# Performance work log

Hardware: AMD Instinct MI355X
Metric: run time of the kernel (lower is better)

The kernel has to match this reference:

```python
import jax, jax.numpy as jnp
import numpy as np

B, S, D, H = 2, 2048, 1024, 16
HD = D // H
EPS = 1e-5


def layer_norm(x, g, b):
    m = jnp.mean(x, axis=-1, keepdims=True)
    v = jnp.mean(jnp.square(x - m), axis=-1, keepdims=True)
    return (x - m) * jax.lax.rsqrt(v + EPS) * g + b


def setup_inputs() -> dict:
    key = jax.random.key(0)
    ks = jax.random.split(key, 16)
    s = 0.02
    x = jax.random.normal(ks[0], (B, S, D), dtype=jnp.float32)
    mask = jax.random.randint(ks[1], (1, 1, S, S), 0, 2, dtype=jnp.int32)
    return {
        "x": x,
        "mask": mask,
        "Wq": jax.random.normal(ks[2], (D, D), jnp.float32) * s,
        "Wk": jax.random.normal(ks[3], (D, D), jnp.float32) * s,
        "Wv": jax.random.normal(ks[4], (D, D), jnp.float32) * s,
        "Wo": jax.random.normal(ks[5], (D, D), jnp.float32) * s,
        "bo": jax.random.normal(ks[6], (D,), jnp.float32) * s,
        "ln1_g": jnp.ones((D,), jnp.float32),
        "ln1_b": jnp.zeros((D,), jnp.float32),
        "W1": jax.random.normal(ks[7], (D, 4 * D), jnp.float32) * s,
        "b1": jax.random.normal(ks[8], (4 * D,), jnp.float32) * s,
        "W2": jax.random.normal(ks[9], (4 * D, D), jnp.float32) * s,
        "b2": jax.random.normal(ks[10], (D,), jnp.float32) * s,
        "ln2_g": jnp.ones((D,), jnp.float32),
        "ln2_b": jnp.zeros((D,), jnp.float32),
    }


def reference(x, mask, Wq, Wk, Wv, Wo, bo, ln1_g, ln1_b, W1, b1, W2, b2, ln2_g, ln2_b):
    # --- multi-head attention (dropout = identity in eval) ---
    q = (x @ Wq).reshape(B, S, H, HD)
    k = (x @ Wk).reshape(B, S, H, HD)
    v = (x @ Wv).reshape(B, S, H, HD)
    scores = jnp.einsum("bshd,bthd->bhst", q, k) / jnp.sqrt(jnp.float32(HD))
    scores = jnp.where(mask == 1, jnp.float32(-1e9), scores)
    p = jax.nn.softmax(scores, axis=-1)
    o = jnp.einsum("bhst,bthd->bshd", p, v).reshape(B, S, D)
    attn_out = o @ Wo + bo
    # --- residual with norm on the branch (note: norm applied to attn output) ---
    x = x + layer_norm(attn_out, ln1_g, ln1_b)
    # --- FFN: gelu after fc1 AND after fc2 (as in source) ---
    h = jax.nn.gelu(x @ W1 + b1, approximate=False)
    h = jax.nn.gelu(h @ W2 + b2, approximate=False)
    x = x + layer_norm(h, ln2_g, ln2_b)
    return x
```

## Files before the change

kernel.cpp:

```cpp
#include <hip/hip_runtime.h>
#include <hip/hip_bf16.h>
#include <cstdint>

#define BB 2
#define SS 2048
#define DD 1024
#define HH 16
#define HDIM 64
#define MROWS (BB*SS)

typedef __bf16 bf16;
using bf16x8 = __bf16 __attribute__((ext_vector_type(8)));
using bf16x4 = __bf16 __attribute__((ext_vector_type(4)));
using bf16x2 = __bf16 __attribute__((ext_vector_type(2)));
using f32x4  = float __attribute__((ext_vector_type(4)));

__device__ __forceinline__ float gelu_exact(float x) {
    return 0.5f * x * (1.f + erff(x * 0.70710678118654752f));
}

__device__ __forceinline__ void stage16(const bf16* g, bf16* lds_chunk_base, int lane) {
#if __has_builtin(__builtin_amdgcn_global_load_lds)
    __builtin_amdgcn_global_load_lds((const __attribute__((address_space(1))) void*)g,
                                     (__attribute__((address_space(3))) void*)lds_chunk_base,
                                     16, 0, 0);
#else
    *(bf16x8*)(lds_chunk_base + lane * 8) = *(const bf16x8*)g;
#endif
}

__device__ __forceinline__ unsigned lds_addr(const void* p) {
    return (unsigned)(uintptr_t)(const __attribute__((address_space(3))) void*)p;
}

__device__ __forceinline__ bf16x8 dsr(unsigned addr) {
    bf16x8 r;
    asm volatile("ds_read_b128 %0, %1" : "=v"(r) : "v"(addr));
    return r;
}

__global__ __launch_bounds__(256) void prep_kernel(
    const float* __restrict__ x, bf16* __restrict__ x_b,
    const int* __restrict__ mask, unsigned long long* __restrict__ maskb,
    const float* __restrict__ Wq, const float* __restrict__ Wk,
    const float* __restrict__ Wv, const float* __restrict__ Wo,
    const float* __restrict__ W1, const float* __restrict__ W2,
    bf16* __restrict__ Wqkv_t, bf16* __restrict__ Wo_t,
    bf16* __restrict__ W1_t, bf16* __restrict__ W2_t) {
    const int bid = blockIdx.x;
    if (bid < 4096) {
        int i = bid * 256 + threadIdx.x;
        float4 v = ((const float4*)x)[i];
        bf16x4 o;
        o[0] = (bf16)v.x; o[1] = (bf16)v.y; o[2] = (bf16)v.z; o[3] = (bf16)v.w;
        *(bf16x4*)(x_b + (size_t)i * 4) = o;
        return;
    }
    if (bid < 20480) {
        int gid = (bid - 4096) * 256 + threadIdx.x;
        int mv = mask[gid];
        unsigned long long bal = __ballot(mv == 1);
        if ((threadIdx.x & 63) == 0) maskb[gid >> 6] = bal;
        return;
    }
    int t = bid - 20480;
    const float* W; bf16* Wt; int K, N, bx, by;
    if (t < 4096) {
        int wsel = t >> 10;
        int tt = t & 1023;
        W  = (wsel == 0) ? Wq : (wsel == 1) ? Wk : (wsel == 2) ? Wv : Wo;
        Wt = (wsel == 3) ? Wo_t : (Wqkv_t + (size_t)wsel * 1024 * 1024);
        K = 1024; N = 1024; bx = (tt & 31) * 32; by = (tt >> 5) * 32;
    } else if (t < 8192) {
        int tt = t - 4096;
        W = W1; Wt = W1_t; K = 1024; N = 4096;
        bx = (tt & 127) * 32; by = (tt >> 7) * 32;
    } else {
        int tt = t - 8192;
        W = W2; Wt = W2_t; K = 4096; N = 1024;
        bx = (tt & 31) * 32; by = (tt >> 5) * 32;
    }
    __shared__ float tile[32][33];
    int tx = threadIdx.x & 31;
    int ty = threadIdx.x >> 5;
#pragma unroll
    for (int j = 0; j < 4; ++j)
        tile[ty + j * 8][tx] = W[(size_t)(by + ty + j * 8) * N + bx + tx];
    __syncthreads();
#pragma unroll
    for (int j = 0; j < 4; ++j)
        Wt[(size_t)(bx + ty + j * 8) * K + by + tx] = (bf16)tile[tx][ty + j * 8];
}

template <int EPI>
__global__ __launch_bounds__(256, 2) void gemm_bt(const bf16* __restrict__ A,
                                                  const bf16* __restrict__ Bt,
                                                  void* __restrict__ C,
                                                  void* __restrict__ C2,
                                                  const float* __restrict__ bias,
                                                  int M, int N, int K, int ldk) {
    __shared__ __align__(16) bf16 As[128 * 64];
    __shared__ __align__(16) bf16 Bs[128 * 64];
    const int tid  = threadIdx.x;
    const int lane = tid & 63;
    const int wave = tid >> 6;
    const int l16  = lane & 15;
    const int quad = lane >> 4;
    const int wm = wave >> 1, wn = wave & 1;

    int bx, by, bz;
    {
        const int Gx = gridDim.x, Gy = gridDim.y, Gz = gridDim.z;
        const int nwg = Gx * Gy * Gz;
        int L = blockIdx.x + Gx * (blockIdx.y + Gy * blockIdx.z);
        if ((nwg & 7) == 0) {
            int chunk = nwg >> 3;
            L = (L & 7) * chunk + (L >> 3);
        }
        bx = L % Gx; int rest = L / Gx; by = rest % Gy; bz = rest / Gy;
    }
    const int m0 = by * 128, n0 = bx * 128;
    const int z  = bz;
    A  += (size_t)z * K;
    Bt += (size_t)z * K;

    f32x4 acc[4][4];
#pragma unroll
    for (int i = 0; i < 4; ++i)
#pragma unroll
        for (int j = 0; j < 4; ++j) acc[i][j] = (f32x4){0.f, 0.f, 0.f, 0.f};

    const int nsteps = K >> 6;
    for (int kt = 0; kt < nsteps; ++kt) {
        const int kbase = kt << 6;
#pragma unroll
        for (int c = 0; c < 4; ++c) {
            int chunk = wave * 4 + c;
            int gi = chunk * 64 + lane;
            int m  = gi >> 3;
            int cp = gi & 7;
            int g  = cp ^ (m & 7);
            stage16(A  + (size_t)(m0 + m) * ldk + kbase + g * 8, As + chunk * 512, lane);
            stage16(Bt + (size_t)(n0 + m) * ldk + kbase + g * 8, Bs + chunk * 512, lane);
        }
        __syncthreads();
#pragma unroll
        for (int ks = 0; ks < 2; ++ks) {
            bf16x8 af[4], bfr[4];
#pragma unroll
            for (int i = 0; i < 4; ++i) {
                int m = wm * 64 + i * 16 + l16;
                int g = ks * 4 + quad;
                af[i]  = *(const bf16x8*)(As + m * 64 + ((g ^ (m & 7)) * 8));
                int n = wn * 64 + i * 16 + l16;
                bfr[i] = *(const bf16x8*)(Bs + n * 64 + ((g ^ (n & 7)) * 8));
            }
#pragma unroll
            for (int i = 0; i < 4; ++i)
#pragma unroll
                for (int j = 0; j < 4; ++j)
                    acc[i][j] = __builtin_amdgcn_mfma_f32_16x16x32_bf16(af[i], bfr[j], acc[i][j], 0, 0, 0);
        }
        __syncthreads();
    }

    float* Cz = (EPI == 4) ? (z ? (float*)C2 : (float*)C) : nullptr;
#pragma unroll
    for (int i = 0; i < 4; ++i) {
        int row = m0 + wm * 64 + i * 16 + quad * 4;
#pragma unroll
        for (int j = 0; j < 4; ++j) {
            int col = n0 + wn * 64 + j * 16 + l16;
            float bv = (EPI == 2) ? bias[col] : 0.f;
#pragma unroll
            for (int r = 0; r < 4; ++r) {
                float v = acc[i][j][r];
                if (EPI == 2) v = gelu_exact(v + bv);
                size_t idx = (size_t)(row + r) * N + col;
                if (EPI == 4) Cz[idx] = v;
                else          ((bf16*)C)[idx] = (bf16)v;
            }
        }
    }
}

template <int EPI>
__global__ __launch_bounds__(512, 2) void gemm256(const bf16* __restrict__ A,
                                                  const bf16* __restrict__ Bt,
                                                  void* __restrict__ C0, void* __restrict__ C1,
                                                  void* __restrict__ C2v, void* __restrict__ C3,
                                                  const float* __restrict__ bias,
                                                  int M, int N, int K, int ldk) {
    __shared__ __align__(16) bf16 As[2 * 16384];
    __shared__ __align__(16) bf16 Bs[2 * 16384];
    const int tid  = threadIdx.x;
    const int lane = tid & 63;
    const int wave = tid >> 6;
    const int l16  = lane & 15;
    const int quad = lane >> 4;
    const int wm = wave >> 2;
    const int wn = wave & 3;

    int bx, by, bz;
    {
        const int Gx = gridDim.x, Gy = gridDim.y, Gz = gridDim.z;
        const int nwg = Gx * Gy * Gz;
        int L = blockIdx.x + Gx * (blockIdx.y + Gy * blockIdx.z);
        if ((nwg & 7) == 0) {
            int chunk = nwg >> 3;
            L = (L & 7) * chunk + (L >> 3);
        }
        bx = L % Gx; int rest = L / Gx; by = rest % Gy; bz = rest / Gy;
    }
    const int m0 = by * 256, n0 = bx * 256;
    const int z  = bz;
    A  += (size_t)z * K;
    Bt += (size_t)z * K;

    const int grow = wave * 8 + (lane >> 3);
    const int gg   = (lane & 7) ^ (grow & 7);
    const bf16* sA = A  + (size_t)(m0 + grow) * ldk + gg * 8;
    const bf16* sB = Bt + (size_t)(n0 + grow) * ldk + gg * 8;
    const int dchunk = wave * 512;

    const unsigned s7 = (unsigned)(l16 & 7);
    const unsigned e0 = ((unsigned)quad ^ s7) * 16;
    const unsigned arow0 = (unsigned)(wm * 128 + l16) * 128;
    const unsigned brow0 = (unsigned)(wn * 64 + l16) * 128;
    const unsigned asBase = lds_addr(As);
    const unsigned bsBase = lds_addr(Bs);

    f32x4 acc[8][4];
#pragma unroll
    for (int i = 0; i < 8; ++i)
#pragma unroll
        for (int j = 0; j < 4; ++j) acc[i][j] = (f32x4){0.f, 0.f, 0.f, 0.f};

    const int nt = K >> 6;

    auto stageHalf = [&](int t, int R0, bool isB) {
        const int kb = t << 6;
        const bf16* s = isB ? sB : sA;
        bf16* d = (isB ? Bs : As) + (t & 1) * 16384 + R0 * 64 + dchunk;
        stage16(s + (size_t)R0 * ldk + kb, d, lane);
        stage16(s + (size_t)(R0 + 64) * ldk + kb, d + 4096, lane);
    };

    stageHalf(0, 0, false); stageHalf(0, 128, false);
    stageHalf(0, 0, true);  stageHalf(0, 128, true);
    if (1 < nt) {
        stageHalf(1, 0, false);
        asm volatile("s_waitcnt vmcnt(2)");
    } else {
        asm volatile("s_waitcnt vmcnt(0)");
    }
    __builtin_amdgcn_s_barrier();

    for (int t = 0; t < nt; ++t) {
        const unsigned ab = asBase + (unsigned)(t & 1) * 32768 + arow0;
        const unsigned bb = bsBase + (unsigned)(t & 1) * 32768 + brow0;
        bf16x8 af[4][2], b0[2][2], b1[2][2];

#pragma unroll
        for (int i = 0; i < 4; ++i) {
            af[i][0] = dsr(ab + i * 2048 + e0);
            af[i][1] = dsr(ab + i * 2048 + (e0 ^ 64));
        }
#pragma unroll
        for (int j = 0; j < 2; ++j) {
            b0[j][0] = dsr(bb + j * 2048 + e0);
            b0[j][1] = dsr(bb + j * 2048 + (e0 ^ 64));
        }
        if (t + 1 < nt) { stageHalf(t + 1, 128, false); stageHalf(t + 1, 0, true); }
        __builtin_amdgcn_s_barrier();
        asm volatile("s_waitcnt lgkmcnt(0)");
        __builtin_amdgcn_sched_barrier(0);
        __builtin_amdgcn_s_setprio(1);
#pragma unroll
        for (int i = 0; i < 4; ++i)
#pragma unroll
            for (int j = 0; j < 2; ++j)
#pragma unroll
                for (int kk = 0; kk < 2; ++kk)
                    acc[i][j] = __builtin_amdgcn_mfma_f32_16x16x32_bf16(af[i][kk], b0[j][kk], acc[i][j], 0, 0, 0);
        __builtin_amdgcn_s_setprio(0);
        __builtin_amdgcn_s_barrier();

#pragma unroll
        for (int j = 0; j < 2; ++j) {
            b1[j][0] = dsr(bb + 4096 + j * 2048 + e0);
            b1[j][1] = dsr(bb + 4096 + j * 2048 + (e0 ^ 64));
        }
        if (t + 1 < nt) stageHalf(t + 1, 128, true);
        __builtin_amdgcn_s_barrier();
        asm volatile("s_waitcnt lgkmcnt(0)");
        __builtin_amdgcn_sched_barrier(0);
        __builtin_amdgcn_s_setprio(1);
#pragma unroll
        for (int i = 0; i < 4; ++i)
#pragma unroll
            for (int j = 0; j < 2; ++j)
#pragma unroll
                for (int kk = 0; kk < 2; ++kk)
                    acc[i][j + 2] = __builtin_amdgcn_mfma_f32_16x16x32_bf16(af[i][kk], b1[j][kk], acc[i][j + 2], 0, 0, 0);
        __builtin_amdgcn_s_setprio(0);
        __builtin_amdgcn_s_barrier();

#pragma unroll
        for (int i = 0; i < 4; ++i) {
            af[i][0] = dsr(ab + 8192 + i * 2048 + e0);
            af[i][1] = dsr(ab + 8192 + i * 2048 + (e0 ^ 64));
        }
        __builtin_amdgcn_s_barrier();
        asm volatile("s_waitcnt lgkmcnt(0)");
        __builtin_amdgcn_sched_barrier(0);
        __builtin_amdgcn_s_setprio(1);
#pragma unroll
        for (int i = 0; i < 4; ++i)
#pragma unroll
            for (int j = 0; j < 2; ++j)
#pragma unroll
                for (int kk = 0; kk < 2; ++kk)
                    acc[i + 4][j + 2] = __builtin_amdgcn_mfma_f32_16x16x32_bf16(af[i][kk], b1[j][kk], acc[i + 4][j + 2], 0, 0, 0);
        __builtin_amdgcn_s_setprio(0);
        __builtin_amdgcn_s_barrier();

        if (t + 2 < nt) stageHalf(t + 2, 0, false);
        __builtin_amdgcn_s_barrier();
        __builtin_amdgcn_s_setprio(1);
#pragma unroll
        for (int i = 0; i < 4; ++i)
#pragma unroll
            for (int j = 0; j < 2; ++j)
#pragma unroll
                for (int kk = 0; kk < 2; ++kk)
                    acc[i + 4][j] = __builtin_amdgcn_mfma_f32_16x16x32_bf16(af[i][kk], b0[j][kk], acc[i + 4][j], 0, 0, 0);
        __builtin_amdgcn_s_setprio(0);
        if (t + 2 < nt) { asm volatile("s_waitcnt vmcnt(2)"); }
        else            { asm volatile("s_waitcnt vmcnt(0)"); }
        __builtin_amdgcn_s_barrier();
    }

    float* Cz = nullptr;
    if (EPI == 4) Cz = (z == 0) ? (float*)C0 : (z == 1) ? (float*)C1 : (z == 2) ? (float*)C2v : (float*)C3;
#pragma unroll
    for (int i = 0; i < 8; ++i) {
        int row = m0 + wm * 128 + i * 16 + quad * 4;
#pragma unroll
        for (int j = 0; j < 4; ++j) {
            int col = n0 + wn * 64 + j * 16 + l16;
            float bv = (EPI == 2) ? bias[col] : 0.f;
#pragma unroll
            for (int r = 0; r < 4; ++r) {
                float v = acc[i][j][r];
                if (EPI == 2) v = gelu_exact(v + bv);
                size_t idx = (size_t)(row + r) * N + col;
                if (EPI == 4) Cz[idx] = v;
                else          ((bf16*)C0)[idx] = (bf16)v;
            }
        }
    }
}

__global__ __launch_bounds__(512, 2) void flash_attn(const bf16* __restrict__ qkv,
                                                     const unsigned long long* __restrict__ maskb,
                                                     bf16* __restrict__ o) {
    __shared__ __align__(16) bf16 Ks[128 * 64];
    __shared__ __align__(16) bf16 Vts[64 * 136];
    const int tid  = threadIdx.x;
    const int lane = tid & 63;
    const int wave = tid >> 6;
    const int l16  = lane & 15;
    const int quad = lane >> 4;

    int bqx, bhy;
    {
        const int Gx = gridDim.x, Gy = gridDim.y;
        int L = blockIdx.x + Gx * blockIdx.y;
        int chunk = (Gx * Gy) >> 3;
        L = (L & 7) * chunk + (L >> 3);
        bqx = L % Gx; bhy = L / Gx;
    }
    const int bh = bhy;
    const int b = bh >> 4, h = bh & 15;
    const int q0 = bqx * 128;
    const size_t rowb = (size_t)b * SS;
    const float SCL = 0.18033688011112042f;

    const size_t qrow = (rowb + q0 + wave * 16 + l16) * 3072 + h * 64;
    bf16x8 qf[2];
    {
        bf16x8 q0r = *(const bf16x8*)(qkv + qrow + quad * 8);
        bf16x8 q1r = *(const bf16x8*)(qkv + qrow + 32 + quad * 8);
#pragma unroll
        for (int j = 0; j < 8; ++j) {
            qf[0][j] = (bf16)((float)q0r[j] * SCL);
            qf[1][j] = (bf16)((float)q1r[j] * SCL);
        }
    }

    f32x4 oacc[4];
#pragma unroll
    for (int d = 0; d < 4; ++d) oacc[d] = (f32x4){0.f, 0.f, 0.f, 0.f};
    f32x4 lacc = (f32x4){0.f, 0.f, 0.f, 0.f};
    const int mrow32 = (q0 + wave * 16 + l16) * 32;

    bf16x8 ones;
#pragma unroll
    for (int j = 0; j < 8; ++j) ones[j] = (bf16)1.0f;

    const int vt_tc = (lane >> 4) * 32 + ((lane >> 1) & 3) * 8 + ((lane >> 3) & 1) * 4 + 2 * (lane & 1);
    const int vd8 = wave * 8;

    int kst[2], ksg[2];
#pragma unroll
    for (int c = 0; c < 2; ++c) {
        int gi = (wave * 2 + c) * 64 + lane;
        kst[c] = gi >> 3;
        ksg[c] = (gi & 7) ^ (kst[c] & 7);
    }

    bf16x8 kreg[2], vreg[2];
    ulonglong2 mwreg;
#pragma unroll
    for (int c = 0; c < 2; ++c)
        kreg[c] = *(const bf16x8*)(qkv + (rowb + kst[c]) * 3072 + 1024 + h * 64 + ksg[c] * 8);
    {
        const bf16* vg = qkv + (rowb + 2 * lane) * 3072 + 2048 + h * 64 + vd8;
        vreg[0] = *(const bf16x8*)(vg);
        vreg[1] = *(const bf16x8*)(vg + 3072);
    }
    mwreg = *(const ulonglong2*)(maskb + mrow32);

    for (int kt = 0; kt < SS / 128; ++kt) {
        __syncthreads();
#pragma unroll
        for (int c = 0; c < 2; ++c)
            *(bf16x8*)(Ks + (wave * 2 + c) * 512 + lane * 8) = kreg[c];
#pragma unroll
        for (int j = 0; j < 8; ++j) {
            bf16x2 pr; pr[0] = vreg[0][j]; pr[1] = vreg[1][j];
            *(bf16x2*)(Vts + (vd8 + j) * 136 + vt_tc) = pr;
        }
        ulonglong2 mw = mwreg;
        __syncthreads();

        if (kt + 1 < SS / 128) {
            const int t0n = (kt + 1) * 128;
#pragma unroll
            for (int c = 0; c < 2; ++c)
                kreg[c] = *(const bf16x8*)(qkv + (rowb + t0n + kst[c]) * 3072 + 1024 + h * 64 + ksg[c] * 8);
            {
                const bf16* vg = qkv + (rowb + t0n + 2 * lane) * 3072 + 2048 + h * 64 + vd8;
                vreg[0] = *(const bf16x8*)(vg);
                vreg[1] = *(const bf16x8*)(vg + 3072);
            }
            mwreg = *(const ulonglong2*)(maskb + mrow32 + (kt + 1) * 2);
        }

        f32x4 st[8];
        __builtin_amdgcn_s_setprio(1);
#pragma unroll
        for (int tg = 0; tg < 8; ++tg) {
            int tl = tg * 16 + l16;
            bf16x8 a0 = *(const bf16x8*)(Ks + tl * 64 + ((quad       ^ (tl & 7)) * 8));
            bf16x8 a1 = *(const bf16x8*)(Ks + tl * 64 + (((4 + quad) ^ (tl & 7)) * 8));
            f32x4 s = (f32x4){0.f, 0.f, 0.f, 0.f};
            s = __builtin_amdgcn_mfma_f32_16x16x32_bf16(a0, qf[0], s, 0, 0, 0);
            s = __builtin_amdgcn_mfma_f32_16x16x32_bf16(a1, qf[1], s, 0, 0, 0);
            st[tg] = s;
        }
        __builtin_amdgcn_s_setprio(0);

        unsigned long long s0 = mw.x >> (quad * 4);
        unsigned long long s1 = mw.y >> (quad * 4);
        bf16x8 pva[4];
#pragma unroll
        for (int tg = 0; tg < 8; ++tg) {
            unsigned int bits = (unsigned int)(((tg < 4) ? s0 : s1) >> ((tg & 3) * 16));
#pragma unroll
            for (int r = 0; r < 4; ++r) {
                float p = __builtin_amdgcn_exp2f(st[tg][r]);
                p = ((bits >> r) & 1u) ? 0.f : p;
                pva[tg >> 1][(tg & 1) * 4 + r] = (bf16)p;
            }
        }

        __builtin_amdgcn_s_setprio(1);
#pragma unroll
        for (int kc = 0; kc < 4; ++kc) {
#pragma unroll
            for (int dg = 0; dg < 4; ++dg) {
                bf16x8 bfrag = *(const bf16x8*)(Vts + (dg * 16 + l16) * 136 + kc * 32 + quad * 8);
                oacc[dg] = __builtin_amdgcn_mfma_f32_16x16x32_bf16(pva[kc], bfrag, oacc[dg], 0, 0, 0);
            }
            lacc = __builtin_amdgcn_mfma_f32_16x16x32_bf16(pva[kc], ones, lacc, 0, 0, 0);
        }
        __builtin_amdgcn_s_setprio(0);
    }

#pragma unroll
    for (int r = 0; r < 4; ++r) {
        float inv_l = 1.f / lacc[r];
        bf16* orow = o + (rowb + q0 + wave * 16 + quad * 4 + r) * DD + h * 64;
#pragma unroll
        for (int dg = 0; dg < 4; ++dg)
            orow[dg * 16 + l16] = (bf16)(oacc[dg][r] * inv_l);
    }
}

template <bool GELU, bool WB16, int NP>
__global__ __launch_bounds__(256) void ln_fused(const float* __restrict__ resid,
                                                const float* __restrict__ p0,
                                                const float* __restrict__ p1,
                                                const float* __restrict__ p2,
                                                const float* __restrict__ p3,
                                                const float* __restrict__ bias,
                                                const float* __restrict__ g,
                                                const float* __restrict__ bb,
                                                float* __restrict__ outf,
                                                bf16* __restrict__ outb) {
    const int row = blockIdx.x;
    const int tid = threadIdx.x;
    const size_t base = (size_t)row * DD + tid * 4;
    float4 a0 = *(const float4*)(p0 + base);
    float4 a1 = *(const float4*)(p1 + base);
    float4 bz = *(const float4*)(bias + tid * 4);
    float ax = a0.x + a1.x + bz.x;
    float ay = a0.y + a1.y + bz.y;
    float az = a0.z + a1.z + bz.z;
    float aw = a0.w + a1.w + bz.w;
    if (NP == 4) {
        float4 a2 = *(const float4*)(p2 + base);
        float4 a3 = *(const float4*)(p3 + base);
        ax += a2.x + a3.x; ay += a2.y + a3.y; az += a2.z + a3.z; aw += a2.w + a3.w;
    }
    if (GELU) { ax = gelu_exact(ax); ay = gelu_exact(ay); az = gelu_exact(az); aw = gelu_exact(aw); }
    float s1 = ax + ay + az + aw;
    float s2 = ax * ax + ay * ay + az * az + aw * aw;
#pragma unroll
    for (int off = 32; off; off >>= 1) {
        s1 += __shfl_xor(s1, off, 64);
        s2 += __shfl_xor(s2, off, 64);
    }
    __shared__ float red[8];
    if ((tid & 63) == 0) { red[(tid >> 6) * 2] = s1; red[(tid >> 6) * 2 + 1] = s2; }
    __syncthreads();
    s1 = red[0] + red[2] + red[4] + red[6];
    s2 = red[1] + red[3] + red[5] + red[7];
    float mean = s1 * (1.f / DD);
    float var  = s2 * (1.f / DD) - mean * mean;
    float rs = rsqrtf(var + 1e-5f);
    float4 gv = *(const float4*)(g + tid * 4);
    float4 bv = *(const float4*)(bb + tid * 4);
    float4 rv = *(const float4*)(resid + base);
    float y0 = rv.x + (ax - mean) * rs * gv.x + bv.x;
    float y1 = rv.y + (ay - mean) * rs * gv.y + bv.y;
    float y2 = rv.z + (az - mean) * rs * gv.z + bv.z;
    float y3 = rv.w + (aw - mean) * rs * gv.w + bv.w;
    float4 yo = make_float4(y0, y1, y2, y3);
    *(float4*)(outf + base) = yo;
    if (WB16) {
        bf16x4 ob;
        ob[0] = (bf16)y0; ob[1] = (bf16)y1; ob[2] = (bf16)y2; ob[3] = (bf16)y3;
        *(bf16x4*)(outb + base) = ob;
    }
}

extern "C" void kernel_launch(void* const* d_in, const int* in_sizes, int n_in,
                              void* d_out, int out_size, void* d_ws, size_t ws_size,
                              hipStream_t stream) {
    const float* x    = (const float*)d_in[0];
    const int*   mask = (const int*)d_in[1];
    const float* Wq   = (const float*)d_in[2];
    const float* Wk   = (const float*)d_in[3];
    const float* Wv   = (const float*)d_in[4];
    const float* Wo   = (const float*)d_in[5];
    const float* bo   = (const float*)d_in[6];
    const float* ln1g = (const float*)d_in[7];
    const float* ln1b = (const float*)d_in[8];
    const float* W1   = (const float*)d_in[9];
    const float* b1   = (const float*)d_in[10];
    const float* W2   = (const float*)d_in[11];
    const float* b2   = (const float*)d_in[12];
    const float* ln2g = (const float*)d_in[13];
    const float* ln2b = (const float*)d_in[14];

    char* w = (char*)d_ws;
    bf16* Wqkv_t = (bf16*)w; w += (size_t)3072 * 1024 * 2;
    bf16* Wo_t   = (bf16*)w; w += (size_t)1024 * 1024 * 2;
    bf16* W1_t   = (bf16*)w; w += (size_t)4096 * 1024 * 2;
    bf16* W2_t   = (bf16*)w; w += (size_t)1024 * 4096 * 2;
    bf16* x_b    = (bf16*)w; w += (size_t)MROWS * DD * 2;
    bf16* qkv    = (bf16*)w; w += (size_t)MROWS * 3072 * 2;
    float* R     = (float*)w; w += (size_t)MROWS * DD * 8;
    float* x1_f  = (float*)w; w += (size_t)MROWS * DD * 4;
    unsigned long long* maskb = (unsigned long long*)w; w += (size_t)SS * 32 * 8;
    bf16* o_b  = x_b;
    bf16* x1_b = x_b;
    float* op0 = R;
    float* op1 = R + (size_t)MROWS * DD;
    bf16*  h_b = (bf16*)R;
    float* fp0 = (float*)d_out;
    float* fp1 = (float*)x_b;
    float* fp2 = (float*)x_b + (size_t)4 * 1024 * 1024;
    float* fp3 = (float*)d_ws;

    prep_kernel<<<32768, 256, 0, stream>>>(x, x_b, mask, maskb,
                                           Wq, Wk, Wv, Wo, W1, W2,
                                           Wqkv_t, Wo_t, W1_t, W2_t);

    gemm256<0><<<dim3(12, 16, 1), 512, 0, stream>>>(x_b, Wqkv_t, qkv, nullptr, nullptr, nullptr, nullptr, MROWS, 3072, 1024, 1024);
    flash_attn<<<dim3(SS / 128, BB * HH), 512, 0, stream>>>(qkv, maskb, o_b);
    gemm_bt<4><<<dim3(8, 32, 2), 256, 0, stream>>>(o_b, Wo_t, op0, op1, nullptr, MROWS, 1024, 512, 1024);
    ln_fused<false, true, 2><<<MROWS, 256, 0, stream>>>(x, op0, op1, nullptr, nullptr, bo, ln1g, ln1b, x1_f, x1_b);
    gemm256<2><<<dim3(16, 16, 1), 512, 0, stream>>>(x1_b, W1_t, h_b, nullptr, nullptr, nullptr, b1, MROWS, 4096, 1024, 1024);
    gemm256<4><<<dim3(4, 16, 4), 512, 0, stream>>>(h_b, W2_t, fp0, fp1, fp2, fp3, nullptr, MROWS, 1024, 1024, 4096);
    ln_fused<true, false, 4><<<MROWS, 256, 0, stream>>>(x1_f, fp0, fp1, fp2, fp3, b2, ln2g, ln2b, (float*)d_out, nullptr);
}
```

Before: 369.4 us.

## Double-buffer K/V shared memory tiles in flash attention to drop a barrier

Gives the K and transposed-V shared tiles two buffers. While computing on tile kt, the kernel writes tile kt+1 into the other buffer and issues global loads for tile kt+2. This cuts the two block barriers per iteration down to one and overlaps the shared-memory stores with compute. In exchange, shared memory per block roughly doubles, which may lower occupancy at 2 blocks of 512 threads per CU, and the loaded register tiles now stay live for longer.

```diff
diff --git a/kernel.cpp b/kernel.cpp
--- a/kernel.cpp
+++ b/kernel.cpp
@@ -365,8 +365,8 @@
 __global__ __launch_bounds__(512, 2) void flash_attn(const bf16* __restrict__ qkv,
                                                      const unsigned long long* __restrict__ maskb,
                                                      bf16* __restrict__ o) {
-    __shared__ __align__(16) bf16 Ks[128 * 64];
-    __shared__ __align__(16) bf16 Vts[64 * 136];
+    __shared__ __align__(16) bf16 Ks[2 * 128 * 64];
+    __shared__ __align__(16) bf16 Vts[2 * 64 * 136];
     const int tid  = threadIdx.x;
     const int lane = tid & 63;
     const int wave = tid >> 6;
@@ -422,49 +422,52 @@
 
     bf16x8 kreg[2], vreg[2];
     ulonglong2 mwreg;
-#pragma unroll
-    for (int c = 0; c < 2; ++c)
-        kreg[c] = *(const bf16x8*)(qkv + (rowb + kst[c]) * 3072 + 1024 + h * 64 + ksg[c] * 8);
-    {
-        const bf16* vg = qkv + (rowb + 2 * lane) * 3072 + 2048 + h * 64 + vd8;
+    auto loadKV = [&](int t0) {
+#pragma unroll
+        for (int c = 0; c < 2; ++c)
+            kreg[c] = *(const bf16x8*)(qkv + (rowb + t0 + kst[c]) * 3072 + 1024 + h * 64 + ksg[c] * 8);
+        const bf16* vg = qkv + (rowb + t0 + 2 * lane) * 3072 + 2048 + h * 64 + vd8;
         vreg[0] = *(const bf16x8*)(vg);
         vreg[1] = *(const bf16x8*)(vg + 3072);
-    }
-    mwreg = *(const ulonglong2*)(maskb + mrow32);
-
-    for (int kt = 0; kt < SS / 128; ++kt) {
-        __syncthreads();
+    };
+    auto commitKV = [&](int buf) {
+        bf16* Ksq = Ks + buf * 8192;
+        bf16* Vtsq = Vts + buf * 8704;
 #pragma unroll
         for (int c = 0; c < 2; ++c)
-            *(bf16x8*)(Ks + (wave * 2 + c) * 512 + lane * 8) = kreg[c];
+            *(bf16x8*)(Ksq + (wave * 2 + c) * 512 + lane * 8) = kreg[c];
 #pragma unroll
         for (int j = 0; j < 8; ++j) {
             bf16x2 pr; pr[0] = vreg[0][j]; pr[1] = vreg[1][j];
-            *(bf16x2*)(Vts + (vd8 + j) * 136 + vt_tc) = pr;
-        }
+            *(bf16x2*)(Vtsq + (vd8 + j) * 136 + vt_tc) = pr;
+        }
+    };
+
+    loadKV(0);
+    mwreg = *(const ulonglong2*)(maskb + mrow32);
+    commitKV(0);
+    loadKV(128);
+    __syncthreads();
+
+    const int NT = SS / 128;
+    for (int kt = 0; kt < NT; ++kt) {
         ulonglong2 mw = mwreg;
-        __syncthreads();
-
-        if (kt + 1 < SS / 128) {
-            const int t0n = (kt + 1) * 128;
-#pragma unroll
-            for (int c = 0; c < 2; ++c)
-                kreg[c] = *(const bf16x8*)(qkv + (rowb + t0n + kst[c]) * 3072 + 1024 + h * 64 + ksg[c] * 8);
-            {
-                const bf16* vg = qkv + (rowb + t0n + 2 * lane) * 3072 + 2048 + h * 64 + vd8;
-                vreg[0] = *(const bf16x8*)(vg);
-                vreg[1] = *(const bf16x8*)(vg + 3072);
-            }
+        if (kt + 1 < NT) {
+            commitKV((kt + 1) & 1);
             mwreg = *(const ulonglong2*)(maskb + mrow32 + (kt + 1) * 2);
-        }
+            if (kt + 2 < NT) loadKV((kt + 2) * 128);
+        }
+
+        const bf16* Ksp = Ks + (kt & 1) * 8192;
+        const bf16* Vtsp = Vts + (kt & 1) * 8704;
 
         f32x4 st[8];
         __builtin_amdgcn_s_setprio(1);
 #pragma unroll
         for (int tg = 0; tg < 8; ++tg) {
             int tl = tg * 16 + l16;
-            bf16x8 a0 = *(const bf16x8*)(Ks + tl * 64 + ((quad       ^ (tl & 7)) * 8));
-            bf16x8 a1 = *(const bf16x8*)(Ks + tl * 64 + (((4 + quad) ^ (tl & 7)) * 8));
+            bf16x8 a0 = *(const bf16x8*)(Ksp + tl * 64 + ((quad       ^ (tl & 7)) * 8));
+            bf16x8 a1 = *(const bf16x8*)(Ksp + tl * 64 + (((4 + quad) ^ (tl & 7)) * 8));
             f32x4 s = (f32x4){0.f, 0.f, 0.f, 0.f};
             s = __builtin_amdgcn_mfma_f32_16x16x32_bf16(a0, qf[0], s, 0, 0, 0);
             s = __builtin_amdgcn_mfma_f32_16x16x32_bf16(a1, qf[1], s, 0, 0, 0);
@@ -491,12 +494,14 @@
         for (int kc = 0; kc < 4; ++kc) {
 #pragma unroll
             for (int dg = 0; dg < 4; ++dg) {
-                bf16x8 bfrag = *(const bf16x8*)(Vts + (dg * 16 + l16) * 136 + kc * 32 + quad * 8);
+                bf16x8 bfrag = *(const bf16x8*)(Vtsp + (dg * 16 + l16) * 136 + kc * 32 + quad * 8);
                 oacc[dg] = __builtin_amdgcn_mfma_f32_16x16x32_bf16(pva[kc], bfrag, oacc[dg], 0, 0, 0);
             }
             lacc = __builtin_amdgcn_mfma_f32_16x16x32_bf16(pva[kc], ones, lacc, 0, 0, 0);
         }
         __builtin_amdgcn_s_setprio(0);
+
+        __syncthreads();
     }
 
 #pragma unroll
```

Result: no change. 372.5 us (+0.8%).
